# Kernel optimization log

Hardware: AMD Instinct MI355X
Metric: run time of the kernel (lower is better)

The kernel has to match this reference:

```python
import jax, jax.numpy as jnp
import numpy as np

B, S, D, H, DFF = 8, 1024, 1024, 16, 4096
DK = D // H
EPS = 1e-5


def layernorm(x, g, b):
    mu = jnp.mean(x, axis=-1, keepdims=True)
    var = jnp.var(x, axis=-1, keepdims=True)
    return (x - mu) * jax.lax.rsqrt(var + EPS) * g + b


def mha(q_in, k_in, v_in, wq, bq, wk, bk, wv, bv, wo, bo):
    # weights stored as [in, out] (transposed torch Linear)
    nb = q_in.shape[0]
    def split(t):  # [B,S,D] -> [B,H,S,DK]
        return t.reshape(nb, -1, H, DK).transpose(0, 2, 1, 3)
    q = split(q_in @ wq + bq)
    k = split(k_in @ wk + bk)
    v = split(v_in @ wv + bv)
    scores = jnp.einsum('bhqd,bhkd->bhqk', q, k) / jnp.sqrt(jnp.float32(DK))
    p = jax.nn.softmax(scores, axis=-1)
    o = jnp.einsum('bhqk,bhkd->bhqd', p, v)
    o = o.transpose(0, 2, 1, 3).reshape(nb, -1, D)
    return o @ wo + bo


def setup_inputs() -> dict:
    key = jax.random.key(0)
    ks = jax.random.split(key, 40)
    i = iter(range(40))
    def rn(shape, scale=1.0):
        return jax.random.normal(ks[next(i)], shape, dtype=jnp.float32) * scale
    d = {}
    d['x'] = rn((B, S, D))
    d['y'] = rn((B, S, D))
    d['x_pos'] = rn((B, S, D))
    d['y_pos'] = rn((B, S, D))
    w_scale = 1.0 / np.sqrt(D)
    for pfx in ('sa', 'ca'):
        for nm in ('q', 'k', 'v', 'o'):
            d[f'{pfx}_w{nm}'] = rn((D, D), w_scale)
            d[f'{pfx}_b{nm}'] = jnp.zeros((D,), jnp.float32)
    d['ffn_w1'] = rn((D, DFF), w_scale)
    d['ffn_b1'] = jnp.zeros((DFF,), jnp.float32)
    d['ffn_w2'] = rn((DFF, D), 1.0 / np.sqrt(DFF))
    d['ffn_b2'] = jnp.zeros((D,), jnp.float32)
    for n in (1, 2, 3, 4):
        d[f'ln{n}_g'] = jnp.ones((D,), jnp.float32)
        d[f'ln{n}_b'] = jnp.zeros((D,), jnp.float32)
    return d


def reference(x, y, x_pos, y_pos,
              sa_wq, sa_bq, sa_wk, sa_bk, sa_wv, sa_bv, sa_wo, sa_bo,
              ca_wq, ca_bq, ca_wk, ca_bk, ca_wv, ca_bv, ca_wo, ca_bo,
              ffn_w1, ffn_b1, ffn_w2, ffn_b2,
              ln1_g, ln1_b, ln2_g, ln2_b, ln3_g, ln3_b, ln4_g, ln4_b):
    # pre-norm variant (norm_before=True), eval mode (dropout=0)
    x2 = layernorm(x, ln1_g, ln1_b)
    qk = x2 + x_pos
    x = x + mha(qk, qk, x2, sa_wq, sa_bq, sa_wk, sa_bk, sa_wv, sa_bv, sa_wo, sa_bo)
    x2 = layernorm(x, ln2_g, ln2_b)
    y2 = layernorm(y, ln3_g, ln3_b)
    x = x + mha(x2 + x_pos, y2 + y_pos, y2,
                ca_wq, ca_bq, ca_wk, ca_bk, ca_wv, ca_bv, ca_wo, ca_bo)
    x2 = layernorm(x, ln4_g, ln4_b)
    h = x2 @ ffn_w1 + ffn_b1
    h = h * jax.nn.sigmoid(h)  # Swish
    return x + (h @ ffn_w2 + ffn_b2)
```

## Files before the change

kernel.cpp:

```cpp
#include <hip/hip_runtime.h>
#include <hip/hip_bf16.h>

#define NB 8
#define NS 1024
#define ND 1024
#define NH 16
#define NDK 64
#define NDFF 4096

typedef __bf16 bf16;
typedef __attribute__((ext_vector_type(8))) __bf16 bf16x8;
typedef __attribute__((ext_vector_type(4))) __bf16 bf16x4;
typedef __attribute__((ext_vector_type(4))) float f32x4;

__device__ __forceinline__ void gload16(const bf16* g, bf16* l) {
  __builtin_amdgcn_global_load_lds(
      (const __attribute__((address_space(1))) void*)g,
      (__attribute__((address_space(3))) void*)l, 16, 0, 0);
}

__global__ void wconv_t(const float* __restrict__ W, bf16* __restrict__ WT,
                        int K, int N) {
  __shared__ float tile[32][33];
  int n0 = blockIdx.x * 32, k0 = blockIdx.y * 32;
  int tx = threadIdx.x, ty = threadIdx.y;
#pragma unroll
  for (int i2 = 0; i2 < 4; ++i2) {
    int i = ty + i2 * 8;
    tile[i][tx] = W[(long)(k0 + i) * N + n0 + tx];
  }
  __syncthreads();
#pragma unroll
  for (int i2 = 0; i2 < 4; ++i2) {
    int i = ty + i2 * 8;
    WT[(long)(n0 + i) * K + k0 + tx] = (bf16)tile[tx][i];
  }
}

struct WPtrs { const float* w[8]; };
__global__ void wconv8(WPtrs wp, bf16* __restrict__ dst) {
  __shared__ float tile[32][33];
  int n0 = blockIdx.x * 32, k0 = blockIdx.y * 32;
  const float* W = wp.w[blockIdx.z];
  bf16* WT = dst + (size_t)blockIdx.z * (1024 * 1024);
  int tx = threadIdx.x, ty = threadIdx.y;
#pragma unroll
  for (int i2 = 0; i2 < 4; ++i2) {
    int i = ty + i2 * 8;
    tile[i][tx] = W[(long)(k0 + i) * 1024 + n0 + tx];
  }
  __syncthreads();
#pragma unroll
  for (int i2 = 0; i2 < 4; ++i2) {
    int i = ty + i2 * 8;
    WT[(long)(n0 + i) * 1024 + k0 + tx] = (bf16)tile[tx][i];
  }
}

__device__ __forceinline__ void ln_body(
    const float* in, const float* gam, const float* bet, const float* pos,
    bf16* out_ln, bf16* out_lnpos, long row) {
  int t = threadIdx.x;
  float4 v = ((const float4*)(in + row * ND))[t];
  float s = v.x + v.y + v.z + v.w;
  float s2 = v.x * v.x + v.y * v.y + v.z * v.z + v.w * v.w;
#pragma unroll
  for (int m = 32; m >= 1; m >>= 1) {
    s += __shfl_xor(s, m);
    s2 += __shfl_xor(s2, m);
  }
  __shared__ float red[8];
  if ((t & 63) == 0) {
    red[t >> 6] = s;
    red[4 + (t >> 6)] = s2;
  }
  __syncthreads();
  float ts = red[0] + red[1] + red[2] + red[3];
  float ts2 = red[4] + red[5] + red[6] + red[7];
  float mu = ts * (1.0f / ND);
  float var = ts2 * (1.0f / ND) - mu * mu;
  float rstd = rsqrtf(var + 1e-5f);
  float4 g4 = ((const float4*)gam)[t];
  float4 b4 = ((const float4*)bet)[t];
  float o0 = (v.x - mu) * rstd * g4.x + b4.x;
  float o1 = (v.y - mu) * rstd * g4.y + b4.y;
  float o2 = (v.z - mu) * rstd * g4.z + b4.z;
  float o3 = (v.w - mu) * rstd * g4.w + b4.w;
  if (out_ln) {
    bf16x4 q;
    q[0] = (bf16)o0; q[1] = (bf16)o1; q[2] = (bf16)o2; q[3] = (bf16)o3;
    *(bf16x4*)(out_ln + row * ND + t * 4) = q;
  }
  if (out_lnpos) {
    float4 p4 = ((const float4*)(pos + row * ND))[t];
    bf16x4 q;
    q[0] = (bf16)(o0 + p4.x); q[1] = (bf16)(o1 + p4.y);
    q[2] = (bf16)(o2 + p4.z); q[3] = (bf16)(o3 + p4.w);
    *(bf16x4*)(out_lnpos + row * ND + t * 4) = q;
  }
}

__global__ void ln_fused(const float* __restrict__ in, const float* __restrict__ gam,
                         const float* __restrict__ bet, const float* __restrict__ pos,
                         bf16* __restrict__ out_ln, bf16* __restrict__ out_lnpos) {
  ln_body(in, gam, bet, pos, out_ln, out_lnpos, blockIdx.x);
}

__global__ void ln_fused2(
    const float* in0, const float* g0, const float* be0, const float* p0,
    bf16* oln0, bf16* olp0,
    const float* in1, const float* g1, const float* be1, const float* p1,
    bf16* oln1, bf16* olp1) {
  int sel = blockIdx.x >> 13;
  long row = blockIdx.x & 8191;
  if (sel == 0)
    ln_body(in0, g0, be0, p0, oln0, olp0, row);
  else
    ln_body(in1, g1, be1, p1, oln1, olp1, row);
}

template <int MODE>
__device__ __forceinline__ void gemm_core(
    const bf16* A, const bf16* WT, const float* bias, const float* res,
    void* out, int N, int K, int mode_rt) {
  __shared__ bf16 SA[3][128 * 32];
  __shared__ bf16 SB[3][128 * 32];
  const int t = threadIdx.x;
  const int w = t >> 6, l = t & 63;
  const int wr = w >> 1, wc = w & 1;
  const int c = l & 15, g = l >> 4;
  const long row0 = (long)blockIdx.x * 128;
  const long col0 = (long)blockIdx.y * 128;
  const int NT = K >> 5;

  f32x4 acc[4][4];
#pragma unroll
  for (int m = 0; m < 4; ++m)
#pragma unroll
    for (int n = 0; n < 4; ++n) acc[m][n] = (f32x4){0.f, 0.f, 0.f, 0.f};

  const int srow = l >> 2;
  const int sslot = 8 * ((l & 3) ^ ((l >> 3) & 3));
  const bf16* Ag0 = A + (row0 + w * 16 + srow) * (long)K + sslot;
  const bf16* Ag1 = Ag0 + 64 * (long)K;
  const bf16* Bg0 = WT + (col0 + w * 16 + srow) * (long)K + sslot;
  const bf16* Bg1 = Bg0 + 64 * (long)K;
  bf16* const SAf = &SA[0][0];
  bf16* const SBf = &SB[0][0];

#define STAGEC(SL, KK)                                           \
  do {                                                           \
    gload16(Ag0 + (KK), SAf + (SL) * 4096 + (w * 16) * 32);      \
    gload16(Ag1 + (KK), SAf + (SL) * 4096 + (64 + w * 16) * 32); \
    gload16(Bg0 + (KK), SBf + (SL) * 4096 + (w * 16) * 32);      \
    gload16(Bg1 + (KK), SBf + (SL) * 4096 + (64 + w * 16) * 32); \
  } while (0)

  STAGEC(0, 0);
  STAGEC(1, 32);

  const int rsw = (g ^ ((c >> 1) & 3)) * 8;
  int aoff[4], boff[4];
#pragma unroll
  for (int m = 0; m < 4; ++m) aoff[m] = (wr * 64 + m * 16 + c) * 32 + rsw;
#pragma unroll
  for (int n = 0; n < 4; ++n) boff[n] = (wc * 64 + n * 16 + c) * 32 + rsw;

  asm volatile("s_waitcnt vmcnt(4)" ::: "memory");
  __builtin_amdgcn_s_barrier();

  int cb = 0, sb = 2, kst = 64;
  for (int tt = 0; tt < NT; ++tt) {
    const int ca = cb * 4096;
    bf16x8 af[4], bfr[4];
#pragma unroll
    for (int m = 0; m < 4; ++m) af[m] = *(const bf16x8*)(SAf + ca + aoff[m]);
#pragma unroll
    for (int n = 0; n < 4; ++n) bfr[n] = *(const bf16x8*)(SBf + ca + boff[n]);

    if (tt + 2 < NT) STAGEC(sb, kst);

    __builtin_amdgcn_s_barrier();
    asm volatile("s_waitcnt lgkmcnt(0)" ::: "memory");
    __builtin_amdgcn_sched_barrier(0);
    __builtin_amdgcn_s_setprio(1);
#pragma unroll
    for (int m = 0; m < 4; ++m)
#pragma unroll
      for (int n = 0; n < 4; ++n)
        acc[m][n] = __builtin_amdgcn_mfma_f32_16x16x32_bf16(af[m], bfr[n], acc[m][n], 0, 0, 0);
    __builtin_amdgcn_s_setprio(0);

    if (tt + 2 < NT) {
      asm volatile("s_waitcnt vmcnt(4)" ::: "memory");
    } else {
      asm volatile("s_waitcnt vmcnt(0)" ::: "memory");
    }
    __builtin_amdgcn_s_barrier();

    cb = (cb == 2) ? 0 : cb + 1;
    sb = (sb == 2) ? 0 : sb + 1;
    kst += 32;
  }
#undef STAGEC

  const int mode = (MODE >= 0) ? MODE : mode_rt;
  if (mode == 3) {
    bf16* VT = (bf16*)out;
#pragma unroll
    for (int n = 0; n < 4; ++n) {
      const long col = col0 + wc * 64 + n * 16 + c;
      const float bv = bias[col];
      const long h = col >> 6, dk = col & 63;
#pragma unroll
      for (int m = 0; m < 4; ++m) {
        const long rowb = row0 + wr * 64 + m * 16 + g * 4;
        const long b = rowb >> 10, s = rowb & 1023;
        bf16x4 ov;
#pragma unroll
        for (int r = 0; r < 4; ++r) ov[r] = (bf16)(acc[m][n][r] + bv);
        *(bf16x4*)(VT + (((b * NH + h) * NDK + dk) << 10) + s) = ov;
      }
    }
    return;
  }

#pragma unroll
  for (int n = 0; n < 4; ++n) {
    const long col = col0 + wc * 64 + n * 16 + c;
    const float bv = bias[col];
#pragma unroll
    for (int m = 0; m < 4; ++m) {
      const long rowb = row0 + wr * 64 + m * 16 + g * 4;
#pragma unroll
      for (int r = 0; r < 4; ++r) {
        float v = acc[m][n][r] + bv;
        const long idx = (rowb + r) * N + col;
        if (mode == 0) {
          ((bf16*)out)[idx] = (bf16)v;
        } else if (mode == 1) {
          ((float*)out)[idx] = res[idx] + v;
        } else {
          float sw = v / (1.f + __expf(-v));
          ((bf16*)out)[idx] = (bf16)sw;
        }
      }
    }
  }
}

template <int MODE>
__global__ __launch_bounds__(256) void gemm_bt(
    const bf16* __restrict__ A, const bf16* __restrict__ WT,
    const float* __restrict__ bias, const float* __restrict__ res,
    void* __restrict__ out, int M, int N, int K) {
  gemm_core<MODE>(A, WT, bias, res, out, N, K, 0);
}

struct GemmJob { const bf16* A; const bf16* WT; const float* bias; void* out; int mode; };
struct Jobs5 { GemmJob j[5]; };
__global__ __launch_bounds__(256) void gemm_multi(Jobs5 jobs) {
  const GemmJob& jb = jobs.j[blockIdx.z];
  gemm_core<-1>(jb.A, jb.WT, jb.bias, nullptr, jb.out, 1024, 1024, jb.mode);
}

template <int MODE>
__global__ __launch_bounds__(512) void gemm_bt8(
    const bf16* __restrict__ A, const bf16* __restrict__ WT,
    const float* __restrict__ bias, const float* __restrict__ res,
    void* __restrict__ out, int M, int N, int K) {
  __shared__ bf16 SA[3][256 * 32];
  __shared__ bf16 SB[3][128 * 32];
  const int t = threadIdx.x;
  const int w = t >> 6, l = t & 63;
  const int wr = w >> 1, wc = w & 1;
  const int c = l & 15, g = l >> 4;
  const long row0 = (long)blockIdx.x * 256;
  const long col0 = (long)blockIdx.y * 128;
  const int NT = K >> 5;

  f32x4 acc[4][4];
#pragma unroll
  for (int m = 0; m < 4; ++m)
#pragma unroll
    for (int n = 0; n < 4; ++n) acc[m][n] = (f32x4){0.f, 0.f, 0.f, 0.f};

  const int srow = l >> 2;
  const int sslot = 8 * ((l & 3) ^ ((l >> 3) & 3));
  const bf16* Ag0 = A + (row0 + w * 16 + srow) * (long)K + sslot;
  const bf16* Ag1 = Ag0 + 128 * (long)K;
  const bf16* Bg0 = WT + (col0 + w * 16 + srow) * (long)K + sslot;
  bf16* const SAf = &SA[0][0];
  bf16* const SBf = &SB[0][0];

#define STAGE8(SL, KK)                                            \
  do {                                                            \
    gload16(Ag0 + (KK), SAf + (SL) * 8192 + (w * 16) * 32);       \
    gload16(Ag1 + (KK), SAf + (SL) * 8192 + (128 + w * 16) * 32); \
    gload16(Bg0 + (KK), SBf + (SL) * 4096 + (w * 16) * 32);       \
  } while (0)

  STAGE8(0, 0);
  STAGE8(1, 32);

  const int rsw = (g ^ ((c >> 1) & 3)) * 8;
  int aoff[4], boff[4];
#pragma unroll
  for (int m = 0; m < 4; ++m) aoff[m] = (wr * 64 + m * 16 + c) * 32 + rsw;
#pragma unroll
  for (int n = 0; n < 4; ++n) boff[n] = (wc * 64 + n * 16 + c) * 32 + rsw;

  asm volatile("s_waitcnt vmcnt(3)" ::: "memory");
  __builtin_amdgcn_s_barrier();

  int cb = 0, sb = 2, kst = 64;
  for (int tt = 0; tt < NT; ++tt) {
    bf16x8 af[4], bfr[4];
#pragma unroll
    for (int m = 0; m < 4; ++m) af[m] = *(const bf16x8*)(SAf + cb * 8192 + aoff[m]);
#pragma unroll
    for (int n = 0; n < 4; ++n) bfr[n] = *(const bf16x8*)(SBf + cb * 4096 + boff[n]);

    if (tt + 2 < NT) STAGE8(sb, kst);

    __builtin_amdgcn_s_barrier();
    asm volatile("s_waitcnt lgkmcnt(0)" ::: "memory");
    __builtin_amdgcn_sched_barrier(0);
    __builtin_amdgcn_s_setprio(1);
#pragma unroll
    for (int m = 0; m < 4; ++m)
#pragma unroll
      for (int n = 0; n < 4; ++n)
        acc[m][n] = __builtin_amdgcn_mfma_f32_16x16x32_bf16(af[m], bfr[n], acc[m][n], 0, 0, 0);
    __builtin_amdgcn_s_setprio(0);

    if (tt + 2 < NT) {
      asm volatile("s_waitcnt vmcnt(3)" ::: "memory");
    } else {
      asm volatile("s_waitcnt vmcnt(0)" ::: "memory");
    }
    __builtin_amdgcn_s_barrier();

    cb = (cb == 2) ? 0 : cb + 1;
    sb = (sb == 2) ? 0 : sb + 1;
    kst += 32;
  }
#undef STAGE8

#pragma unroll
  for (int n = 0; n < 4; ++n) {
    const long col = col0 + wc * 64 + n * 16 + c;
    const float bv = bias[col];
#pragma unroll
    for (int m = 0; m < 4; ++m) {
      const long rowb = row0 + wr * 64 + m * 16 + g * 4;
#pragma unroll
      for (int r = 0; r < 4; ++r) {
        float v = acc[m][n][r] + bv;
        const long idx = (rowb + r) * N + col;
        if (MODE == 0) {
          ((bf16*)out)[idx] = (bf16)v;
        } else if (MODE == 1) {
          ((float*)out)[idx] = res[idx] + v;
        } else {
          float sw = v / (1.f + __expf(-v));
          ((bf16*)out)[idx] = (bf16)sw;
        }
      }
    }
  }
}

__global__ __launch_bounds__(512) void attn_fwd(
    const bf16* __restrict__ Q, const bf16* __restrict__ Kt,
    const bf16* __restrict__ VT, bf16* __restrict__ O) {
  __shared__ bf16 Ks[2][64 * 64];
  __shared__ bf16 Vs[2][64 * 64];
  __shared__ bf16 Pl[8][2][16 * 68];
  int t = threadIdx.x;
  int w = t >> 6, l = t & 63;
  int c = l & 15, g = l >> 4;
  int bid = blockIdx.x;
  int qt = bid >> 7, bh = bid & 127;
  int b = bh >> 4, h = bh & 15;
  int q0 = qt * 256 + w * 32;
  int swz = (c & 7) << 4;

  bf16x8 qf[2][2];
  const bf16* Qbase = Q + (long)(b * NS) * ND + h * NDK;
#pragma unroll
  for (int sj = 0; sj < 2; ++sj) {
    const bf16* qr = Qbase + (long)(q0 + sj * 16 + c) * ND + g * 8;
    qf[sj][0] = *(const bf16x8*)qr;
    qf[sj][1] = *(const bf16x8*)(qr + 32);
  }

  const bf16* Kg = Kt + (long)(b * NS) * ND + h * NDK;
  const bf16* Vg = VT + (long)(b * NH + h) * NDK * NS;

  int sr = l >> 3;
  int sc8 = 8 * ((l & 7) ^ sr);

  f32x4 o[2][4];
#pragma unroll
  for (int sj = 0; sj < 2; ++sj)
#pragma unroll
    for (int ds = 0; ds < 4; ++ds) o[sj][ds] = (f32x4){0.f, 0.f, 0.f, 0.f};
  float mx[2] = {-1e30f, -1e30f};
  float lsum[2] = {0.f, 0.f};

#define STAGEA(BUF, KV)                                                       \
  {                                                                           \
    int row = w * 8 + sr;                                                     \
    gload16(Kg + (long)((KV) + row) * ND + sc8, &Ks[BUF][(w * 8) * 64]);      \
    gload16(Vg + (long)row * NS + (KV) + sc8, &Vs[BUF][(w * 8) * 64]);        \
  }

  STAGEA(0, 0);

  int buf = 0;
  for (int it = 0; it < NS / 64; ++it) {
    if (it + 1 < NS / 64) {
      STAGEA(buf ^ 1, (it + 1) * 64);
      asm volatile("s_waitcnt vmcnt(2)" ::: "memory");
    } else {
      asm volatile("s_waitcnt vmcnt(0)" ::: "memory");
    }
    __builtin_amdgcn_s_barrier();

    f32x4 sv[2][4];
#pragma unroll
    for (int sj = 0; sj < 2; ++sj)
#pragma unroll
      for (int kt = 0; kt < 4; ++kt) sv[sj][kt] = (f32x4){0.f, 0.f, 0.f, 0.f};
    __builtin_amdgcn_s_setprio(1);
#pragma unroll
    for (int kt = 0; kt < 4; ++kt) {
      const char* kr = (const char*)&Ks[buf][(kt * 16 + c) * 64];
      bf16x8 ka0 = *(const bf16x8*)(kr + ((g * 16) ^ swz));
      bf16x8 ka1 = *(const bf16x8*)(kr + ((64 + g * 16) ^ swz));
#pragma unroll
      for (int sj = 0; sj < 2; ++sj) {
        sv[sj][kt] = __builtin_amdgcn_mfma_f32_16x16x32_bf16(ka0, qf[sj][0], sv[sj][kt], 0, 0, 0);
        sv[sj][kt] = __builtin_amdgcn_mfma_f32_16x16x32_bf16(ka1, qf[sj][1], sv[sj][kt], 0, 0, 0);
      }
    }
    __builtin_amdgcn_s_setprio(0);

    float pm[2];
#pragma unroll
    for (int sj = 0; sj < 2; ++sj) {
      float m = -1e30f;
#pragma unroll
      for (int kt = 0; kt < 4; ++kt)
#pragma unroll
        for (int r = 0; r < 4; ++r) {
          sv[sj][kt][r] *= 0.125f;
          m = fmaxf(m, sv[sj][kt][r]);
        }
      m = fmaxf(m, __shfl_xor(m, 16));
      m = fmaxf(m, __shfl_xor(m, 32));
      pm[sj] = m;
    }
    int cond = (pm[0] <= mx[0] + 8.f) && (pm[1] <= mx[1] + 8.f);
    if (!__all(cond)) {
#pragma unroll
      for (int sj = 0; sj < 2; ++sj) {
        float mn = fmaxf(mx[sj], pm[sj]);
        float sc = __expf(mx[sj] - mn);
        mx[sj] = mn;
        lsum[sj] *= sc;
#pragma unroll
        for (int ds = 0; ds < 4; ++ds)
#pragma unroll
          for (int r = 0; r < 4; ++r) o[sj][ds][r] *= sc;
      }
    }
#pragma unroll
    for (int sj = 0; sj < 2; ++sj) {
      float rs = 0.f;
#pragma unroll
      for (int kt = 0; kt < 4; ++kt) {
        bf16x4 pw;
#pragma unroll
        for (int r = 0; r < 4; ++r) {
          float e = __expf(sv[sj][kt][r] - mx[sj]);
          rs += e;
          pw[r] = (bf16)e;
        }
        *(bf16x4*)&Pl[w][sj][c * 68 + kt * 16 + 4 * g] = pw;
      }
      rs += __shfl_xor(rs, 16);
      rs += __shfl_xor(rs, 32);
      lsum[sj] += rs;
    }
    asm volatile("s_waitcnt lgkmcnt(0)" ::: "memory");
    __builtin_amdgcn_sched_barrier(0);

    __builtin_amdgcn_s_setprio(1);
#pragma unroll
    for (int ks = 0; ks < 2; ++ks) {
      bf16x8 pb0 = *(const bf16x8*)&Pl[w][0][c * 68 + ks * 32 + g * 8];
      bf16x8 pb1 = *(const bf16x8*)&Pl[w][1][c * 68 + ks * 32 + g * 8];
#pragma unroll
      for (int ds = 0; ds < 4; ++ds) {
        const char* vr = (const char*)&Vs[buf][(ds * 16 + c) * 64];
        bf16x8 va = *(const bf16x8*)(vr + ((ks * 64 + g * 16) ^ swz));
        o[0][ds] = __builtin_amdgcn_mfma_f32_16x16x32_bf16(va, pb0, o[0][ds], 0, 0, 0);
        o[1][ds] = __builtin_amdgcn_mfma_f32_16x16x32_bf16(va, pb1, o[1][ds], 0, 0, 0);
      }
    }
    __builtin_amdgcn_s_setprio(0);
    __builtin_amdgcn_s_barrier();
    buf ^= 1;
  }

#pragma unroll
  for (int sj = 0; sj < 2; ++sj) {
    float inv = 1.f / lsum[sj];
    bf16* Orow = O + (long)(b * NS + q0 + sj * 16 + c) * ND + h * NDK;
#pragma unroll
    for (int ds = 0; ds < 4; ++ds) {
      bf16x4 ov;
#pragma unroll
      for (int r = 0; r < 4; ++r) ov[r] = (bf16)(o[sj][ds][r] * inv);
      *(bf16x4*)(Orow + ds * 16 + 4 * g) = ov;
    }
  }
#undef STAGEA
}

extern "C" void kernel_launch(void* const* d_in, const int* in_sizes, int n_in,
                              void* d_out, int out_size, void* d_ws, size_t ws_size,
                              hipStream_t stream) {
  (void)in_sizes; (void)n_in; (void)out_size; (void)ws_size;
  const float* x = (const float*)d_in[0];
  const float* y = (const float*)d_in[1];
  const float* x_pos = (const float*)d_in[2];
  const float* y_pos = (const float*)d_in[3];

  char* ws = (char*)d_ws;
  const size_t MB = 1ull << 20;
  bf16* Wt[8];
  for (int i = 0; i < 8; ++i) Wt[i] = (bf16*)(ws + (size_t)i * 2 * MB);
  bf16* W1T = (bf16*)(ws + 16 * MB);
  bf16* W2T = (bf16*)(ws + 24 * MB);
  float* xres = (float*)(ws + 32 * MB);
  bf16* x2 = (bf16*)(ws + 64 * MB);
  bf16* qk = (bf16*)(ws + 80 * MB);
  bf16* y2 = (bf16*)(ws + 96 * MB);
  bf16* yk = (bf16*)(ws + 112 * MB);
  bf16* Qb = (bf16*)(ws + 128 * MB);
  bf16* Kb = (bf16*)(ws + 144 * MB);
  bf16* Kb2 = (bf16*)(ws + 160 * MB);
  bf16* VTb = (bf16*)(ws + 176 * MB);
  bf16* Ob = (bf16*)(ws + 192 * MB);
  bf16* VTb2 = (bf16*)(ws + 208 * MB);
  bf16* hb = (bf16*)(ws + 128 * MB);

  dim3 tb(32, 8);
  WPtrs wp;
  for (int i = 0; i < 8; ++i) wp.w[i] = (const float*)d_in[4 + 2 * i];
  wconv8<<<dim3(32, 32, 8), tb, 0, stream>>>(wp, (bf16*)ws);
  wconv_t<<<dim3(128, 32), tb, 0, stream>>>((const float*)d_in[20], W1T, 1024, 4096);
  wconv_t<<<dim3(32, 128), tb, 0, stream>>>((const float*)d_in[22], W2T, 4096, 1024);

  const float* ln1g = (const float*)d_in[24]; const float* ln1b = (const float*)d_in[25];
  const float* ln2g = (const float*)d_in[26]; const float* ln2b = (const float*)d_in[27];
  const float* ln3g = (const float*)d_in[28]; const float* ln3b = (const float*)d_in[29];
  const float* ln4g = (const float*)d_in[30]; const float* ln4b = (const float*)d_in[31];

  dim3 gD(64, 8);
  dim3 gQKV(64, 8, 5);
  dim3 gF1(32, 32);

  ln_fused2<<<16384, 256, 0, stream>>>(x, ln1g, ln1b, x_pos, x2, qk,
                                       y, ln3g, ln3b, y_pos, y2, yk);

  Jobs5 jobs;
  jobs.j[0] = {qk, Wt[0], (const float*)d_in[5], Qb, 0};
  jobs.j[1] = {qk, Wt[1], (const float*)d_in[7], Kb, 0};
  jobs.j[2] = {x2, Wt[2], (const float*)d_in[9], VTb, 3};
  jobs.j[3] = {yk, Wt[5], (const float*)d_in[15], Kb2, 0};
  jobs.j[4] = {y2, Wt[6], (const float*)d_in[17], VTb2, 3};
  gemm_multi<<<gQKV, 256, 0, stream>>>(jobs);

  attn_fwd<<<512, 512, 0, stream>>>(Qb, Kb, VTb, Ob);
  gemm_bt<1><<<gD, 256, 0, stream>>>(Ob, Wt[3], (const float*)d_in[11], x, xres, 8192, 1024, 1024);

  ln_fused<<<8192, 256, 0, stream>>>(xres, ln2g, ln2b, x_pos, nullptr, qk);
  gemm_bt<0><<<gD, 256, 0, stream>>>(qk, Wt[4], (const float*)d_in[13], nullptr, Qb, 8192, 1024, 1024);
  attn_fwd<<<512, 512, 0, stream>>>(Qb, Kb2, VTb2, Ob);
  gemm_bt<1><<<gD, 256, 0, stream>>>(Ob, Wt[7], (const float*)d_in[19], xres, xres, 8192, 1024, 1024);

  ln_fused<<<8192, 256, 0, stream>>>(xres, ln4g, ln4b, nullptr, x2, nullptr);
  gemm_bt8<2><<<gF1, 512, 0, stream>>>(x2, W1T, (const float*)d_in[21], nullptr, hb, 8192, 4096, 1024);
  gemm_bt<1><<<gD, 256, 0, stream>>>(hb, W2T, (const float*)d_in[23], xres, (float*)d_out, 8192, 1024, 4096);
}
```

Baseline: 617.3 us.

## Triple-buffer attention K/V staging and merge weight conversions into one launch

The attention kernel moves from two to three LDS buffers for K/V tiles and prefetches two tiles ahead, waiting with vmcnt(4) so each tile's global-to-LDS loads have more time to land before use. Separately, the three weight-transpose/convert kernels become a single launch that dispatches on a flat block index, removing two kernel launches. The deeper pipeline raises LDS use per block, which may reduce occupancy.

```diff
diff --git a/kernel.cpp b/kernel.cpp
--- a/kernel.cpp
+++ b/kernel.cpp
@@ -19,10 +19,27 @@
       (__attribute__((address_space(3))) void*)l, 16, 0, 0);
 }
 
-__global__ void wconv_t(const float* __restrict__ W, bf16* __restrict__ WT,
-                        int K, int N) {
+struct WAll { const float* w[10]; };
+__global__ void wconv_all(WAll wp, bf16* __restrict__ dst8,
+                          bf16* __restrict__ W1T, bf16* __restrict__ W2T) {
   __shared__ float tile[32][33];
-  int n0 = blockIdx.x * 32, k0 = blockIdx.y * 32;
+  const int j = blockIdx.x;
+  const float* W;
+  bf16* WT;
+  int K, N, n0, k0;
+  if (j < 8192) {
+    int wi = j >> 10, r = j & 1023;
+    W = wp.w[wi]; WT = dst8 + (size_t)wi * (1024 * 1024);
+    K = 1024; N = 1024; n0 = (r & 31) * 32; k0 = (r >> 5) * 32;
+  } else if (j < 12288) {
+    int r = j - 8192;
+    W = wp.w[8]; WT = W1T; K = 1024; N = 4096;
+    n0 = (r & 127) * 32; k0 = (r >> 7) * 32;
+  } else {
+    int r = j - 12288;
+    W = wp.w[9]; WT = W2T; K = 4096; N = 1024;
+    n0 = (r & 31) * 32; k0 = (r >> 5) * 32;
+  }
   int tx = threadIdx.x, ty = threadIdx.y;
 #pragma unroll
   for (int i2 = 0; i2 < 4; ++i2) {
@@ -34,26 +51,6 @@
   for (int i2 = 0; i2 < 4; ++i2) {
     int i = ty + i2 * 8;
     WT[(long)(n0 + i) * K + k0 + tx] = (bf16)tile[tx][i];
-  }
-}
-
-struct WPtrs { const float* w[8]; };
-__global__ void wconv8(WPtrs wp, bf16* __restrict__ dst) {
-  __shared__ float tile[32][33];
-  int n0 = blockIdx.x * 32, k0 = blockIdx.y * 32;
-  const float* W = wp.w[blockIdx.z];
-  bf16* WT = dst + (size_t)blockIdx.z * (1024 * 1024);
-  int tx = threadIdx.x, ty = threadIdx.y;
-#pragma unroll
-  for (int i2 = 0; i2 < 4; ++i2) {
-    int i = ty + i2 * 8;
-    tile[i][tx] = W[(long)(k0 + i) * 1024 + n0 + tx];
-  }
-  __syncthreads();
-#pragma unroll
-  for (int i2 = 0; i2 < 4; ++i2) {
-    int i = ty + i2 * 8;
-    WT[(long)(n0 + i) * 1024 + k0 + tx] = (bf16)tile[tx][i];
   }
 }
 
@@ -374,8 +371,8 @@
 __global__ __launch_bounds__(512) void attn_fwd(
     const bf16* __restrict__ Q, const bf16* __restrict__ Kt,
     const bf16* __restrict__ VT, bf16* __restrict__ O) {
-  __shared__ bf16 Ks[2][64 * 64];
-  __shared__ bf16 Vs[2][64 * 64];
+  __shared__ bf16 Ks[3][64 * 64];
+  __shared__ bf16 Vs[3][64 * 64];
   __shared__ bf16 Pl[8][2][16 * 68];
   int t = threadIdx.x;
   int w = t >> 6, l = t & 63;
@@ -417,11 +414,15 @@
   }
 
   STAGEA(0, 0);
+  STAGEA(1, 64);
 
   int buf = 0;
   for (int it = 0; it < NS / 64; ++it) {
-    if (it + 1 < NS / 64) {
-      STAGEA(buf ^ 1, (it + 1) * 64);
+    if (it + 2 < NS / 64) {
+      int sb = (buf == 0) ? 2 : (buf - 1);
+      STAGEA(sb, (it + 2) * 64);
+      asm volatile("s_waitcnt vmcnt(4)" ::: "memory");
+    } else if (it + 1 < NS / 64) {
       asm volatile("s_waitcnt vmcnt(2)" ::: "memory");
     } else {
       asm volatile("s_waitcnt vmcnt(0)" ::: "memory");
@@ -512,7 +513,7 @@
     }
     __builtin_amdgcn_s_setprio(0);
     __builtin_amdgcn_s_barrier();
-    buf ^= 1;
+    buf = (buf == 2) ? 0 : buf + 1;
   }
 
 #pragma unroll
@@ -559,11 +560,11 @@
   bf16* hb = (bf16*)(ws + 128 * MB);
 
   dim3 tb(32, 8);
-  WPtrs wp;
-  for (int i = 0; i < 8; ++i) wp.w[i] = (const float*)d_in[4 + 2 * i];
-  wconv8<<<dim3(32, 32, 8), tb, 0, stream>>>(wp, (bf16*)ws);
-  wconv_t<<<dim3(128, 32), tb, 0, stream>>>((const float*)d_in[20], W1T, 1024, 4096);
-  wconv_t<<<dim3(32, 128), tb, 0, stream>>>((const float*)d_in[22], W2T, 4096, 1024);
+  WAll wa;
+  for (int i = 0; i < 8; ++i) wa.w[i] = (const float*)d_in[4 + 2 * i];
+  wa.w[8] = (const float*)d_in[20];
+  wa.w[9] = (const float*)d_in[22];
+  wconv_all<<<16384, tb, 0, stream>>>(wa, (bf16*)ws, W1T, W2T);
 
   const float* ln1g = (const float*)d_in[24]; const float* ln1b = (const float*)d_in[25];
   const float* ln2g = (const float*)d_in[26]; const float* ln2b = (const float*)d_in[27];
```

After: 643.7 us. 1.04x slower.

## Enlarge FFN1 GEMM tile to 256x256 with split B-fragment loads

Applied to the files above, without the earlier changes.

The FFN up-projection GEMM changes from 256x128 to 256x256 block tiles. Each wave now computes a 128x64 sub-tile with 8x4 accumulators, and the grid is halved. The main loop is restructured so B fragments load in two halves, with the A and B global-to-LDS prefetches placed between the two MFMA groups, and the wait/barrier moves to the top of the iteration. This is meant to raise arithmetic intensity and overlap loads with compute, at the cost of more accumulator registers, more LDS, and only 512 blocks.

```diff
diff --git a/kernel.cpp b/kernel.cpp
--- a/kernel.cpp
+++ b/kernel.cpp
@@ -265,23 +265,23 @@
 }
 
 template <int MODE>
-__global__ __launch_bounds__(512) void gemm_bt8(
+__global__ __launch_bounds__(512) void gemm256(
     const bf16* __restrict__ A, const bf16* __restrict__ WT,
-    const float* __restrict__ bias, const float* __restrict__ res,
-    void* __restrict__ out, int M, int N, int K) {
+    const float* __restrict__ bias, void* __restrict__ out, int N, int K) {
   __shared__ bf16 SA[3][256 * 32];
-  __shared__ bf16 SB[3][128 * 32];
+  __shared__ bf16 SB[3][256 * 32];
   const int t = threadIdx.x;
   const int w = t >> 6, l = t & 63;
-  const int wr = w >> 1, wc = w & 1;
+  const int wr = w >> 2;
+  const int wcn = w & 3;
   const int c = l & 15, g = l >> 4;
   const long row0 = (long)blockIdx.x * 256;
-  const long col0 = (long)blockIdx.y * 128;
+  const long col0 = (long)blockIdx.y * 256;
   const int NT = K >> 5;
 
-  f32x4 acc[4][4];
-#pragma unroll
-  for (int m = 0; m < 4; ++m)
+  f32x4 acc[8][4];
+#pragma unroll
+  for (int m = 0; m < 8; ++m)
 #pragma unroll
     for (int n = 0; n < 4; ++n) acc[m][n] = (f32x4){0.f, 0.f, 0.f, 0.f};
 
@@ -290,78 +290,92 @@
   const bf16* Ag0 = A + (row0 + w * 16 + srow) * (long)K + sslot;
   const bf16* Ag1 = Ag0 + 128 * (long)K;
   const bf16* Bg0 = WT + (col0 + w * 16 + srow) * (long)K + sslot;
+  const bf16* Bg1 = Bg0 + 128 * (long)K;
   bf16* const SAf = &SA[0][0];
   bf16* const SBf = &SB[0][0];
 
-#define STAGE8(SL, KK)                                            \
+#define SGA(SL, KK)                                               \
   do {                                                            \
     gload16(Ag0 + (KK), SAf + (SL) * 8192 + (w * 16) * 32);       \
     gload16(Ag1 + (KK), SAf + (SL) * 8192 + (128 + w * 16) * 32); \
-    gload16(Bg0 + (KK), SBf + (SL) * 4096 + (w * 16) * 32);       \
   } while (0)
-
-  STAGE8(0, 0);
-  STAGE8(1, 32);
+#define SGB(SL, KK)                                               \
+  do {                                                            \
+    gload16(Bg0 + (KK), SBf + (SL) * 8192 + (w * 16) * 32);       \
+    gload16(Bg1 + (KK), SBf + (SL) * 8192 + (128 + w * 16) * 32); \
+  } while (0)
+
+  SGA(0, 0); SGB(0, 0);
+  SGA(1, 32); SGB(1, 32);
 
   const int rsw = (g ^ ((c >> 1) & 3)) * 8;
-  int aoff[4], boff[4];
-#pragma unroll
-  for (int m = 0; m < 4; ++m) aoff[m] = (wr * 64 + m * 16 + c) * 32 + rsw;
-#pragma unroll
-  for (int n = 0; n < 4; ++n) boff[n] = (wc * 64 + n * 16 + c) * 32 + rsw;
-
-  asm volatile("s_waitcnt vmcnt(3)" ::: "memory");
-  __builtin_amdgcn_s_barrier();
+  int aoff[8], boff[4];
+#pragma unroll
+  for (int m = 0; m < 8; ++m) aoff[m] = (wr * 128 + m * 16 + c) * 32 + rsw;
+#pragma unroll
+  for (int n = 0; n < 4; ++n) boff[n] = (wcn * 64 + n * 16 + c) * 32 + rsw;
 
   int cb = 0, sb = 2, kst = 64;
   for (int tt = 0; tt < NT; ++tt) {
-    bf16x8 af[4], bfr[4];
-#pragma unroll
-    for (int m = 0; m < 4; ++m) af[m] = *(const bf16x8*)(SAf + cb * 8192 + aoff[m]);
-#pragma unroll
-    for (int n = 0; n < 4; ++n) bfr[n] = *(const bf16x8*)(SBf + cb * 4096 + boff[n]);
-
-    if (tt + 2 < NT) STAGE8(sb, kst);
-
+    if (tt + 1 < NT) {
+      asm volatile("s_waitcnt vmcnt(4)" ::: "memory");
+    } else {
+      asm volatile("s_waitcnt vmcnt(0)" ::: "memory");
+    }
     __builtin_amdgcn_s_barrier();
+
+    const int ca = cb * 8192;
+    const bool st = (tt + 2) < NT;
+
+    bf16x8 af[8], bf0, bf1;
+#pragma unroll
+    for (int m = 0; m < 8; ++m) af[m] = *(const bf16x8*)(SAf + ca + aoff[m]);
+    bf0 = *(const bf16x8*)(SBf + ca + boff[0]);
+    bf1 = *(const bf16x8*)(SBf + ca + boff[1]);
+    if (st) SGA(sb, kst);
     asm volatile("s_waitcnt lgkmcnt(0)" ::: "memory");
     __builtin_amdgcn_sched_barrier(0);
     __builtin_amdgcn_s_setprio(1);
 #pragma unroll
-    for (int m = 0; m < 4; ++m)
-#pragma unroll
-      for (int n = 0; n < 4; ++n)
-        acc[m][n] = __builtin_amdgcn_mfma_f32_16x16x32_bf16(af[m], bfr[n], acc[m][n], 0, 0, 0);
+    for (int m = 0; m < 8; ++m) {
+      acc[m][0] = __builtin_amdgcn_mfma_f32_16x16x32_bf16(af[m], bf0, acc[m][0], 0, 0, 0);
+      acc[m][1] = __builtin_amdgcn_mfma_f32_16x16x32_bf16(af[m], bf1, acc[m][1], 0, 0, 0);
+    }
     __builtin_amdgcn_s_setprio(0);
 
-    if (tt + 2 < NT) {
-      asm volatile("s_waitcnt vmcnt(3)" ::: "memory");
-    } else {
-      asm volatile("s_waitcnt vmcnt(0)" ::: "memory");
-    }
-    __builtin_amdgcn_s_barrier();
+    bf16x8 bf2 = *(const bf16x8*)(SBf + ca + boff[2]);
+    bf16x8 bf3 = *(const bf16x8*)(SBf + ca + boff[3]);
+    if (st) SGB(sb, kst);
+    asm volatile("s_waitcnt lgkmcnt(0)" ::: "memory");
+    __builtin_amdgcn_sched_barrier(0);
+    __builtin_amdgcn_s_setprio(1);
+#pragma unroll
+    for (int m = 0; m < 8; ++m) {
+      acc[m][2] = __builtin_amdgcn_mfma_f32_16x16x32_bf16(af[m], bf2, acc[m][2], 0, 0, 0);
+      acc[m][3] = __builtin_amdgcn_mfma_f32_16x16x32_bf16(af[m], bf3, acc[m][3], 0, 0, 0);
+    }
+    __builtin_amdgcn_s_setprio(0);
 
     cb = (cb == 2) ? 0 : cb + 1;
     sb = (sb == 2) ? 0 : sb + 1;
     kst += 32;
   }
-#undef STAGE8
+#undef SGA
+#undef SGB
 
 #pragma unroll
   for (int n = 0; n < 4; ++n) {
-    const long col = col0 + wc * 64 + n * 16 + c;
+    const long col = col0 + wcn * 64 + n * 16 + c;
     const float bv = bias[col];
 #pragma unroll
-    for (int m = 0; m < 4; ++m) {
-      const long rowb = row0 + wr * 64 + m * 16 + g * 4;
+    for (int m = 0; m < 8; ++m) {
+      const long rowb = row0 + wr * 128 + m * 16 + g * 4;
 #pragma unroll
       for (int r = 0; r < 4; ++r) {
         float v = acc[m][n][r] + bv;
         const long idx = (rowb + r) * N + col;
         if (MODE == 0) {
           ((bf16*)out)[idx] = (bf16)v;
-        } else if (MODE == 1) {
-          ((float*)out)[idx] = res[idx] + v;
         } else {
           float sw = v / (1.f + __expf(-v));
           ((bf16*)out)[idx] = (bf16)sw;
@@ -572,7 +586,7 @@
 
   dim3 gD(64, 8);
   dim3 gQKV(64, 8, 5);
-  dim3 gF1(32, 32);
+  dim3 gF1(32, 16);
 
   ln_fused2<<<16384, 256, 0, stream>>>(x, ln1g, ln1b, x_pos, x2, qk,
                                        y, ln3g, ln3b, y_pos, y2, yk);
@@ -594,6 +608,6 @@
   gemm_bt<1><<<gD, 256, 0, stream>>>(Ob, Wt[7], (const float*)d_in[19], xres, xres, 8192, 1024, 1024);
 
   ln_fused<<<8192, 256, 0, stream>>>(xres, ln4g, ln4b, nullptr, x2, nullptr);
-  gemm_bt8<2><<<gF1, 512, 0, stream>>>(x2, W1T, (const float*)d_in[21], nullptr, hb, 8192, 4096, 1024);
+  gemm256<2><<<gF1, 512, 0, stream>>>(x2, W1T, (const float*)d_in[21], hb, 4096, 1024);
   gemm_bt<1><<<gD, 256, 0, stream>>>(hb, W2T, (const float*)d_in[23], xres, (float*)d_out, 8192, 1024, 4096);
 }
```

Result: no change. 621.4 us (+0.7%).
